# Kernel optimization log

Hardware: AMD Instinct MI355X
Metric: run time of the kernel (lower is better)

Reference implementation:

```python
import jax, jax.numpy as jnp
import numpy as np

NUM_HEADS = 16
ROPE_THETA = 10000.0


def apply_rope(x):
    # x: (B, H, T, hd), interleaved-pair RoPE (rotary-embedding-torch convention)
    T, hd = x.shape[-2], x.shape[-1]
    inv_freq = 1.0 / (ROPE_THETA ** (jnp.arange(0, hd, 2, dtype=jnp.float32) / hd))  # (hd/2,)
    ang = jnp.arange(T, dtype=jnp.float32)[:, None] * inv_freq[None, :]  # (T, hd/2)
    cos, sin = jnp.cos(ang), jnp.sin(ang)
    x1 = x[..., 0::2]
    x2 = x[..., 1::2]
    r1 = x1 * cos - x2 * sin
    r2 = x1 * sin + x2 * cos
    return jnp.stack([r1, r2], axis=-1).reshape(x.shape)


def setup_inputs() -> dict:
    key = jax.random.key(0)
    ks = jax.random.split(key, 8)
    L, S, B, E = 2048, 2048, 2, 1024
    sc = 1.0 / np.sqrt(E)
    return {
        "query": jax.random.normal(ks[0], (L, B, E), jnp.float32),
        "key": jax.random.normal(ks[1], (S, B, E), jnp.float32),
        "value": jax.random.normal(ks[2], (S, B, E), jnp.float32),
        "key_padding_mask": jnp.zeros((B, S), dtype=bool),
        "Wq": jax.random.normal(ks[3], (E, E), jnp.float32) * sc,
        "bq": jnp.zeros((E,), jnp.float32),
        "Wk": jax.random.normal(ks[4], (E, E), jnp.float32) * sc,
        "bk": jnp.zeros((E,), jnp.float32),
        "Wv": jax.random.normal(ks[5], (E, E), jnp.float32) * sc,
        "bv": jnp.zeros((E,), jnp.float32),
        "Wo": jax.random.normal(ks[6], (E, E), jnp.float32) * sc,
        "bo": jnp.zeros((E,), jnp.float32),
    }


def reference(query, key, value, key_padding_mask, Wq, bq, Wk, bk, Wv, bv, Wo, bo):
    L, B, E = query.shape
    S = key.shape[0]
    H = NUM_HEADS
    hd = E // H
    # projections (torch Linear: x @ W.T + b)
    Q = query @ Wq.T + bq  # (L, B, E)
    K = key @ Wk.T + bk    # (S, B, E)
    V = value @ Wv.T + bv  # (S, B, E)
    # (T, B, E) -> (B, H, T, hd)
    Q = Q.reshape(L, B, H, hd).transpose(1, 2, 0, 3)
    K = K.reshape(S, B, H, hd).transpose(1, 2, 0, 3)
    V = V.reshape(S, B, H, hd).transpose(1, 2, 0, 3)
    Q = apply_rope(Q)
    K = apply_rope(K)
    scores = jnp.einsum("bhld,bhsd->bhls", Q, K) / jnp.sqrt(jnp.float32(hd))
    scores = jnp.where(key_padding_mask[:, None, None, :], -jnp.inf, scores)
    attn = jax.nn.softmax(scores, axis=-1)
    out = jnp.einsum("bhls,bhsd->bhld", attn, V)  # (B, H, L, hd)
    out = out.transpose(2, 0, 1, 3).reshape(L, B, E)
    return out @ Wo.T + bo
```

## Files before the change

### kernel.cpp

```cpp
#include <hip/hip_runtime.h>
#include <hip/hip_bf16.h>

typedef __hip_bfloat16 bf16;
typedef short bf16x8 __attribute__((ext_vector_type(8)));
typedef float f32x4 __attribute__((ext_vector_type(4)));
typedef short s4 __attribute__((ext_vector_type(4)));

#define LL 2048
#define SS 2048
#define EE 1024
#define HH 16
#define HD 64
#define MM (LL * 2)

static __device__ __forceinline__ short f2bs(float f) {
  bf16 h = __float2bfloat16(f);
  short u;
  __builtin_memcpy(&u, &h, 2);
  return u;
}

#define GLL16(gp, lp) __builtin_amdgcn_global_load_lds(                        \
    (const __attribute__((address_space(1))) void*)(gp),                       \
    (__attribute__((address_space(3))) void*)(lp), 16, 0, 0)

__global__ __launch_bounds__(256) void tables_kernel(
    float2* __restrict__ tab, const unsigned char* __restrict__ m,
    float* __restrict__ mf) {
  if (blockIdx.x < 256) {
    int i = blockIdx.x * 256 + threadIdx.x;
    int pos = i >> 5, fi = i & 31;
    float freq = expf(-(float)fi * (9.210340371976184f / 32.0f));
    float ang = (float)pos * freq;
    float s, c;
    sincosf(ang, &s, &c);
    tab[i] = make_float2(c, s);
  } else {
    int i = (blockIdx.x - 256) * 256 + threadIdx.x;
    if (i < 2 * SS) mf[i] = m[i] ? -1e30f : 0.f;
  }
}

__global__ __launch_bounds__(256) void cvt_kernel(const float* __restrict__ src,
                                                  bf16* __restrict__ dst) {
  size_t i = ((size_t)blockIdx.x * 256 + threadIdx.x) * 4;
  float4 v = *(const float4*)(src + i);
  s4 p;
  p[0] = f2bs(v.x); p[1] = f2bs(v.y); p[2] = f2bs(v.z); p[3] = f2bs(v.w);
  *(s4*)(dst + i) = p;
}

__global__ __launch_bounds__(256) void cvt4_kernel(
    const float* __restrict__ s0, const float* __restrict__ s1,
    const float* __restrict__ s2, const float* __restrict__ s3,
    bf16* __restrict__ dst) {
  int sel = blockIdx.x >> 10;
  const float* src = (sel == 0) ? s0 : (sel == 1) ? s1 : (sel == 2) ? s2 : s3;
  size_t loc = ((size_t)(blockIdx.x & 1023) * 256 + threadIdx.x) * 4;
  float4 v = *(const float4*)(src + loc);
  s4 p;
  p[0] = f2bs(v.x); p[1] = f2bs(v.y); p[2] = f2bs(v.z); p[3] = f2bs(v.w);
  *(s4*)(dst + (size_t)sel * EE * EE + loc) = p;
}

template<int MODE, bool XB16, bool WB16>
__global__ __launch_bounds__(256) void proj_kernel(
    const void* __restrict__ Xv, const void* __restrict__ Wv,
    const float* __restrict__ bias, void* __restrict__ dstv,
    const float2* __restrict__ tab)
{
  const int w = threadIdx.x >> 6;
  const int lane = threadIdx.x & 63;
  const int l15 = lane & 15, quad = lane >> 4;
  const int tm = blockIdx.x * 128 + w * 32;
  const int tn = blockIdx.y * 64;

  const size_t aoff0 = (size_t)(tm + l15) * EE + quad * 8;
  const size_t aoff1 = aoff0 + (size_t)16 * EE;
  const size_t woff  = (size_t)(tn + l15) * EE + quad * 8;

  f32x4 zero4 = {0.f, 0.f, 0.f, 0.f};
  f32x4 acc[2][4];
#pragma unroll
  for (int mi = 0; mi < 2; ++mi)
#pragma unroll
    for (int ni = 0; ni < 4; ++ni) acc[mi][ni] = zero4;

  for (int k0 = 0; k0 < EE; k0 += 32) {
    bf16x8 a0, a1;
    if (XB16 || MODE == 3) {
      const bf16* Xb = (const bf16*)Xv;
      a0 = *(const bf16x8*)(Xb + aoff0 + k0);
      a1 = *(const bf16x8*)(Xb + aoff1 + k0);
    } else {
      const float* Xf = (const float*)Xv;
#pragma unroll
      for (int j = 0; j < 8; ++j) a0[j] = f2bs(Xf[aoff0 + k0 + j]);
#pragma unroll
      for (int j = 0; j < 8; ++j) a1[j] = f2bs(Xf[aoff1 + k0 + j]);
    }
#pragma unroll
    for (int ni = 0; ni < 4; ++ni) {
      bf16x8 bv;
      if (WB16) {
        const bf16* Wb = (const bf16*)Wv;
        bv = *(const bf16x8*)(Wb + woff + (size_t)ni * 16 * EE + k0);
      } else {
        const float* Wf = (const float*)Wv;
#pragma unroll
        for (int j = 0; j < 8; ++j) bv[j] = f2bs(Wf[woff + (size_t)ni * 16 * EE + k0 + j]);
      }
      acc[0][ni] = __builtin_amdgcn_mfma_f32_16x16x32_bf16(a0, bv, acc[0][ni], 0, 0, 0);
      acc[1][ni] = __builtin_amdgcn_mfma_f32_16x16x32_bf16(a1, bv, acc[1][ni], 0, 0, 0);
    }
  }

  float bz[4];
#pragma unroll
  for (int ni = 0; ni < 4; ++ni) bz[ni] = bias[tn + ni * 16 + l15];

#pragma unroll
  for (int mi = 0; mi < 2; ++mi) {
#pragma unroll
    for (int ni = 0; ni < 4; ++ni) {
      const int n = tn + ni * 16 + l15;
#pragma unroll
      for (int r = 0; r < 4; ++r) {
        const int m = tm + mi * 16 + quad * 4 + r;
        float v = acc[mi][ni][r] + bz[ni];
        if (MODE <= 1) {
          float other = __shfl_xor(v, 1, 64);
          int pos = m >> 1, b = m & 1, d = n & 63, h = n >> 6;
          float2 cs = tab[pos * 32 + (d >> 1)];
          float rv = (d & 1) ? (other * cs.y + v * cs.x) : (v * cs.x - other * cs.y);
          ((bf16*)dstv)[((size_t)(b * HH + h) * LL + pos) * HD + d] = __float2bfloat16(rv);
        } else if (MODE == 2) {
          int pos = m >> 1, b = m & 1, d = n & 63, h = n >> 6;
          ((bf16*)dstv)[((size_t)(b * HH + h) * HD + d) * SS + pos] = __float2bfloat16(v);
        } else {
          ((float*)dstv)[(size_t)m * EE + n] = v;
        }
      }
    }
  }
}

template<int MODE>
__global__ __launch_bounds__(256) void projs_kernel(
    const bf16* __restrict__ X, const bf16* __restrict__ W,
    const float* __restrict__ bias, void* __restrict__ dstv,
    const float2* __restrict__ tab)
{
  __shared__ __align__(16) bf16 As[2][128 * 64];
  __shared__ __align__(16) bf16 Bs[2][64 * 64];

  const int tid = threadIdx.x;
  const int w = tid >> 6;
  const int lane = tid & 63;
  const int l15 = lane & 15, quad = lane >> 4;
  const int tmb = blockIdx.x * 128;
  const int tm  = tmb + w * 32;
  const int tn  = blockIdx.y * 64;

  const int srow = lane >> 3;
  const int sgc  = ((lane & 7) ^ srow) * 8;

#define PSTAGE(buf, K0) {                                                      \
    _Pragma("unroll")                                                          \
    for (int i = 0; i < 4; ++i) {                                              \
      const int rb = w * 32 + i * 8;                                           \
      GLL16(X + (size_t)(tmb + rb + srow) * EE + (K0) + sgc,                   \
            (bf16*)&As[buf][rb * 64] + lane * 8);                              \
    }                                                                          \
    _Pragma("unroll")                                                          \
    for (int i = 0; i < 2; ++i) {                                              \
      const int rb = w * 16 + i * 8;                                           \
      GLL16(W + (size_t)(tn + rb + srow) * EE + (K0) + sgc,                    \
            (bf16*)&Bs[buf][rb * 64] + lane * 8);                              \
    }                                                                          \
  }

  f32x4 zero4 = {0.f, 0.f, 0.f, 0.f};
  f32x4 acc[2][4];
#pragma unroll
  for (int mi = 0; mi < 2; ++mi)
#pragma unroll
    for (int ni = 0; ni < 4; ++ni) acc[mi][ni] = zero4;

  PSTAGE(0, 0);
  __syncthreads();

  for (int t = 0; t < EE / 64; ++t) {
    const int cur = t & 1;
    if (t + 1 < EE / 64) PSTAGE(cur ^ 1, (t + 1) * 64);
#pragma unroll
    for (int ks = 0; ks < 2; ++ks) {
      const int rsw = ((ks * 4 + quad) ^ (l15 & 7)) * 8;
      bf16x8 a0 = *(const bf16x8*)(&As[cur][0] + (w * 32 + l15) * 64 + rsw);
      bf16x8 a1 = *(const bf16x8*)(&As[cur][0] + (w * 32 + 16 + l15) * 64 + rsw);
#pragma unroll
      for (int ni = 0; ni < 4; ++ni) {
        bf16x8 bfr = *(const bf16x8*)(&Bs[cur][0] + (ni * 16 + l15) * 64 + rsw);
        acc[0][ni] = __builtin_amdgcn_mfma_f32_16x16x32_bf16(a0, bfr, acc[0][ni], 0, 0, 0);
        acc[1][ni] = __builtin_amdgcn_mfma_f32_16x16x32_bf16(a1, bfr, acc[1][ni], 0, 0, 0);
      }
    }
    __syncthreads();
  }
#undef PSTAGE

  float bz[4];
#pragma unroll
  for (int ni = 0; ni < 4; ++ni) bz[ni] = bias[tn + ni * 16 + l15];

#pragma unroll
  for (int mi = 0; mi < 2; ++mi) {
#pragma unroll
    for (int ni = 0; ni < 4; ++ni) {
      const int n = tn + ni * 16 + l15;
#pragma unroll
      for (int r = 0; r < 4; ++r) {
        const int m = tm + mi * 16 + quad * 4 + r;
        float v = acc[mi][ni][r] + bz[ni];
        if (MODE <= 1) {
          float other = __shfl_xor(v, 1, 64);
          int pos = m >> 1, b = m & 1, d = n & 63, h = n >> 6;
          float2 cs = tab[pos * 32 + (d >> 1)];
          float rv = (d & 1) ? (other * cs.y + v * cs.x) : (v * cs.x - other * cs.y);
          ((bf16*)dstv)[((size_t)(b * HH + h) * LL + pos) * HD + d] = __float2bfloat16(rv);
        } else if (MODE == 2) {
          int pos = m >> 1, b = m & 1, d = n & 63, h = n >> 6;
          ((bf16*)dstv)[((size_t)(b * HH + h) * HD + d) * SS + pos] = __float2bfloat16(v);
        } else {
          ((float*)dstv)[(size_t)m * EE + n] = v;
        }
      }
    }
  }
}

__global__ __launch_bounds__(256) void attn_kernel(
    const bf16* __restrict__ Qr, const bf16* __restrict__ Kr,
    const bf16* __restrict__ Vt, const float* __restrict__ maskf,
    bf16* __restrict__ ctx)
{
  __shared__ __align__(16) bf16 Ks[2][64 * 64];
  __shared__ __align__(16) bf16 Vs[2][64 * 64];
  __shared__ __align__(16) short Plds[4][32][56];

  const int w = threadIdx.x >> 6;
  const int lane = threadIdx.x & 63;
  const int l15 = lane & 15, quad = lane >> 4;
  const int id = blockIdx.x;
  const int bh = id & 31;
  const int qt = id >> 5;
  const int b = bh >> 4, h = bh & 15;
  const int q0 = qt * 128 + w * 32;

  const bf16* Qbh = Qr + (size_t)bh * LL * HD;
  const bf16* Kbh = Kr + (size_t)bh * SS * HD;
  const bf16* Vbh = Vt + (size_t)bh * HD * SS;
  const float* mrow = maskf + b * SS;

  bf16x8 qf[2][2];
#pragma unroll
  for (int mi = 0; mi < 2; ++mi) {
    const bf16* qp = Qbh + (size_t)(q0 + mi * 16 + l15) * HD + quad * 8;
    qf[mi][0] = *(const bf16x8*)(qp);
    qf[mi][1] = *(const bf16x8*)(qp + 32);
  }

  const int srow = lane >> 3;
  const int gswz = ((lane & 7) ^ srow) * 8;
  const int kswz0 = ((quad    ) ^ (l15 & 7)) * 8;
  const int kswz1 = ((quad + 4) ^ (l15 & 7)) * 8;

#define STAGE(buf, S0) {                                                       \
    _Pragma("unroll")                                                          \
    for (int i = 0; i < 2; ++i) {                                              \
      const int rb = w * 16 + i * 8;                                           \
      GLL16(Kbh + (size_t)((S0) + rb + srow) * HD + gswz,                      \
            (bf16*)&Ks[buf][rb * 64] + lane * 8);                              \
      GLL16(Vbh + (size_t)(rb + srow) * SS + (S0) + gswz,                      \
            (bf16*)&Vs[buf][rb * 64] + lane * 8);                              \
    }                                                                          \
  }

  f32x4 zero4 = {0.f, 0.f, 0.f, 0.f};
  f32x4 o[2][4];
#pragma unroll
  for (int mi = 0; mi < 2; ++mi)
#pragma unroll
    for (int t = 0; t < 4; ++t) o[mi][t] = zero4;
  float ps0 = 0.f, ps1 = 0.f;

  STAGE(0, 0);
  __syncthreads();

  for (int t = 0; t < SS / 64; ++t) {
    const int s0 = t * 64;
    const int cur = t & 1;
    if (t + 1 < SS / 64) STAGE(cur ^ 1, s0 + 64);

#pragma unroll
    for (int ss = 0; ss < 2; ++ss) {
      const bf16* Kb = &Ks[cur][ss * 32 * 64];
      bf16x8 kf00 = *(const bf16x8*)(Kb + (l15)      * 64 + kswz0);
      bf16x8 kf01 = *(const bf16x8*)(Kb + (l15)      * 64 + kswz1);
      bf16x8 kf10 = *(const bf16x8*)(Kb + (16 + l15) * 64 + kswz0);
      bf16x8 kf11 = *(const bf16x8*)(Kb + (16 + l15) * 64 + kswz1);
      bf16x8 vf[4];
#pragma unroll
      for (int tt = 0; tt < 4; ++tt)
        vf[tt] = *(const bf16x8*)(&Vs[cur][0] + (tt * 16 + l15) * 64 +
                                  (((ss * 4 + quad) ^ (l15 & 7)) * 8));
      f32x4 mv0 = *(const f32x4*)(mrow + s0 + ss * 32 + quad * 4);
      f32x4 mv1 = *(const f32x4*)(mrow + s0 + ss * 32 + 16 + quad * 4);

#pragma unroll
      for (int mi = 0; mi < 2; ++mi) {
        f32x4 sc0 = zero4, sc1 = zero4;
        sc0 = __builtin_amdgcn_mfma_f32_16x16x32_bf16(kf00, qf[mi][0], sc0, 0, 0, 0);
        sc0 = __builtin_amdgcn_mfma_f32_16x16x32_bf16(kf01, qf[mi][1], sc0, 0, 0, 0);
        sc1 = __builtin_amdgcn_mfma_f32_16x16x32_bf16(kf10, qf[mi][0], sc1, 0, 0, 0);
        sc1 = __builtin_amdgcn_mfma_f32_16x16x32_bf16(kf11, qf[mi][1], sc1, 0, 0, 0);
        s4 pk0, pk1;
#pragma unroll
        for (int r = 0; r < 4; ++r) {
          float p = __expf(sc0[r] * 0.125f + mv0[r]);
          if (mi == 0) ps0 += p; else ps1 += p;
          pk0[r] = f2bs(p);
        }
#pragma unroll
        for (int r = 0; r < 4; ++r) {
          float p = __expf(sc1[r] * 0.125f + mv1[r]);
          if (mi == 0) ps0 += p; else ps1 += p;
          pk1[r] = f2bs(p);
        }
        *(s4*)&Plds[w][mi * 16 + l15][quad * 4] = pk0;
        *(s4*)&Plds[w][mi * 16 + l15][16 + quad * 4] = pk1;
      }
      asm volatile("" ::: "memory");
      bf16x8 pf0 = *(const bf16x8*)&Plds[w][l15][quad * 8];
      bf16x8 pf1 = *(const bf16x8*)&Plds[w][16 + l15][quad * 8];
#pragma unroll
      for (int tt = 0; tt < 4; ++tt) {
        o[0][tt] = __builtin_amdgcn_mfma_f32_16x16x32_bf16(pf0, vf[tt], o[0][tt], 0, 0, 0);
        o[1][tt] = __builtin_amdgcn_mfma_f32_16x16x32_bf16(pf1, vf[tt], o[1][tt], 0, 0, 0);
      }
      asm volatile("" ::: "memory");
    }
    __syncthreads();
  }
#undef STAGE

  float lv0 = ps0; lv0 += __shfl_xor(lv0, 16, 64); lv0 += __shfl_xor(lv0, 32, 64);
  float lv1 = ps1; lv1 += __shfl_xor(lv1, 16, 64); lv1 += __shfl_xor(lv1, 32, 64);

#pragma unroll
  for (int mi = 0; mi < 2; ++mi) {
#pragma unroll
    for (int r = 0; r < 4; ++r) {
      float lv = (mi == 0) ? lv0 : lv1;
      float li = __shfl(lv, quad * 4 + r, 64);
      float inv = 1.0f / li;
      int q = q0 + mi * 16 + quad * 4 + r;
#pragma unroll
      for (int t = 0; t < 4; ++t) {
        float val = o[mi][t][r] * inv;
        ctx[(size_t)(q * 2 + b) * EE + (size_t)h * 64 + t * 16 + l15] = __float2bfloat16(val);
      }
    }
  }
}

extern "C" void kernel_launch(void* const* d_in, const int* in_sizes, int n_in,
                              void* d_out, int out_size, void* d_ws, size_t ws_size,
                              hipStream_t stream) {
  const float* query = (const float*)d_in[0];
  const float* key   = (const float*)d_in[1];
  const float* value = (const float*)d_in[2];
  const unsigned char* mask = (const unsigned char*)d_in[3];
  const float* Wq = (const float*)d_in[4];
  const float* bq = (const float*)d_in[5];
  const float* Wk = (const float*)d_in[6];
  const float* bk = (const float*)d_in[7];
  const float* Wv = (const float*)d_in[8];
  const float* bv = (const float*)d_in[9];
  const float* Wo = (const float*)d_in[10];
  const float* bo = (const float*)d_in[11];

  char* ws = (char*)d_ws;
  const bool big = ws_size >= ((size_t)41 << 20);

  float2* tab   = (float2*)ws;
  float*  maskf = (float*)(ws + (512 << 10));
  bf16* Wb = (bf16*)(ws + ((size_t)1 << 20));
  bf16* Xb = (bf16*)(ws + ((size_t)9 << 20));
  size_t base = big ? ((size_t)17 << 20) : ((size_t)1 << 20);
  bf16* Qr  = (bf16*)(ws + base);
  bf16* Kr  = (bf16*)(ws + base + ((size_t)8 << 20));
  bf16* Vt  = (bf16*)(ws + base + ((size_t)16 << 20));
  bf16* ctx = big ? Xb : (bf16*)(ws + ((size_t)25 << 20));

  tables_kernel<<<272, 256, 0, stream>>>(tab, mask, maskf);

  dim3 gp(MM / 128, EE / 64);
  if (big) {
    cvt4_kernel<<<4096, 256, 0, stream>>>(Wq, Wk, Wv, Wo, Wb);
    cvt_kernel<<<4096, 256, 0, stream>>>(query, Xb);
    projs_kernel<0><<<gp, 256, 0, stream>>>(Xb, Wb, bq, Qr, tab);
    cvt_kernel<<<4096, 256, 0, stream>>>(key, Xb);
    projs_kernel<1><<<gp, 256, 0, stream>>>(Xb, Wb + (size_t)EE * EE, bk, Kr, tab);
    cvt_kernel<<<4096, 256, 0, stream>>>(value, Xb);
    projs_kernel<2><<<gp, 256, 0, stream>>>(Xb, Wb + (size_t)2 * EE * EE, bv, Vt, tab);
  } else {
    proj_kernel<0, false, false><<<gp, 256, 0, stream>>>(query, Wq, bq, Qr, tab);
    proj_kernel<1, false, false><<<gp, 256, 0, stream>>>(key,   Wk, bk, Kr, tab);
    proj_kernel<2, false, false><<<gp, 256, 0, stream>>>(value, Wv, bv, Vt, tab);
  }

  attn_kernel<<<(LL / 128) * 2 * HH, 256, 0, stream>>>(Qr, Kr, Vt, maskf, ctx);

  if (big) projs_kernel<3><<<gp, 256, 0, stream>>>(ctx, Wb + (size_t)3 * EE * EE, bo, d_out, tab);
  else     proj_kernel<3, true, false><<<gp, 256, 0, stream>>>(ctx, Wo, bo, d_out, tab);
}
```

Measured before the change: 265.9 us.

## Fuse fp32-to-bf16 input conversion into a single batched QKV projection kernel

Removes the three separate activation conversion kernels and instead loads fp32 activations directly in the projection, converting to bf16 in registers before storing to LDS. The Q, K and V projections are merged into one 1536-block launch, with K-tile 32 and a launch bound targeting higher occupancy. The output projection gets a new kernel with 64x64 tiles for more blocks. This trades fewer launches and no intermediate bf16 buffer round trip against register-staged fp32 loads, unswizzled LDS layouts that may bank-conflict, and smaller K steps with more barriers.

After: 261.7 us. No clear change (-1.6%).

```diff
diff --git a/kernel.cpp b/kernel.cpp
--- a/kernel.cpp
+++ b/kernel.cpp
@@ -18,6 +18,13 @@
   short u;
   __builtin_memcpy(&u, &h, 2);
   return u;
+}
+
+static __device__ __forceinline__ void st8(bf16* p, float4 x, float4 y) {
+  bf16x8 v;
+  v[0] = f2bs(x.x); v[1] = f2bs(x.y); v[2] = f2bs(x.z); v[3] = f2bs(x.w);
+  v[4] = f2bs(y.x); v[5] = f2bs(y.y); v[6] = f2bs(y.z); v[7] = f2bs(y.w);
+  *(bf16x8*)p = v;
 }
 
 #define GLL16(gp, lp) __builtin_amdgcn_global_load_lds(                        \
@@ -39,15 +46,6 @@
     int i = (blockIdx.x - 256) * 256 + threadIdx.x;
     if (i < 2 * SS) mf[i] = m[i] ? -1e30f : 0.f;
   }
-}
-
-__global__ __launch_bounds__(256) void cvt_kernel(const float* __restrict__ src,
-                                                  bf16* __restrict__ dst) {
-  size_t i = ((size_t)blockIdx.x * 256 + threadIdx.x) * 4;
-  float4 v = *(const float4*)(src + i);
-  s4 p;
-  p[0] = f2bs(v.x); p[1] = f2bs(v.y); p[2] = f2bs(v.z); p[3] = f2bs(v.w);
-  *(s4*)(dst + i) = p;
 }
 
 __global__ __launch_bounds__(256) void cvt4_kernel(
@@ -145,40 +143,37 @@
   }
 }
 
-template<int MODE>
-__global__ __launch_bounds__(256) void projs_kernel(
-    const bf16* __restrict__ X, const bf16* __restrict__ W,
-    const float* __restrict__ bias, void* __restrict__ dstv,
+__global__ __launch_bounds__(256, 4) void qkv_kernel(
+    const float* __restrict__ Xq, const float* __restrict__ Xk,
+    const float* __restrict__ Xv, const bf16* __restrict__ Wb,
+    const float* __restrict__ bq, const float* __restrict__ bk,
+    const float* __restrict__ bv, bf16* __restrict__ Qr,
+    bf16* __restrict__ Kr, bf16* __restrict__ Vt,
     const float2* __restrict__ tab)
 {
-  __shared__ __align__(16) bf16 As[2][128 * 64];
-  __shared__ __align__(16) bf16 Bs[2][64 * 64];
+  __shared__ __align__(16) bf16 As[2][128 * 32];
+  __shared__ __align__(16) bf16 Bs[2][64 * 32];
 
   const int tid = threadIdx.x;
   const int w = tid >> 6;
   const int lane = tid & 63;
   const int l15 = lane & 15, quad = lane >> 4;
-  const int tmb = blockIdx.x * 128;
-  const int tm  = tmb + w * 32;
-  const int tn  = blockIdx.y * 64;
-
-  const int srow = lane >> 3;
-  const int sgc  = ((lane & 7) ^ srow) * 8;
-
-#define PSTAGE(buf, K0) {                                                      \
-    _Pragma("unroll")                                                          \
-    for (int i = 0; i < 4; ++i) {                                              \
-      const int rb = w * 32 + i * 8;                                           \
-      GLL16(X + (size_t)(tmb + rb + srow) * EE + (K0) + sgc,                   \
-            (bf16*)&As[buf][rb * 64] + lane * 8);                              \
-    }                                                                          \
-    _Pragma("unroll")                                                          \
-    for (int i = 0; i < 2; ++i) {                                              \
-      const int rb = w * 16 + i * 8;                                           \
-      GLL16(W + (size_t)(tn + rb + srow) * EE + (K0) + sgc,                    \
-            (bf16*)&Bs[buf][rb * 64] + lane * 8);                              \
-    }                                                                          \
-  }
+  const int id = blockIdx.x;
+  const int z = id >> 9;
+  const int g = id & 511;
+  const int tmb = (g & 31) * 128;
+  const int tn  = (g >> 5) * 64;
+
+  const float* Xf = (z == 0) ? Xq : (z == 1) ? Xk : Xv;
+  const bf16* Wm  = Wb + (size_t)z * EE * EE;
+  const float* bias = (z == 0) ? bq : (z == 1) ? bk : bv;
+  bf16* dst = (z == 0) ? Qr : (z == 1) ? Kr : Vt;
+
+  const int ar = tid >> 2;
+  const int ac = (tid & 3) * 8;
+  const float* gA0 = Xf + (size_t)(tmb + ar) * EE + ac;
+  const float* gA1 = gA0 + (size_t)64 * EE;
+  const bf16* gB = Wm + (size_t)(tn + w * 16 + (lane >> 2)) * EE + (lane & 3) * 8;
 
   f32x4 zero4 = {0.f, 0.f, 0.f, 0.f};
   f32x4 acc[2][4];
@@ -187,27 +182,42 @@
 #pragma unroll
     for (int ni = 0; ni < 4; ++ni) acc[mi][ni] = zero4;
 
-  PSTAGE(0, 0);
+  {
+    float4 a00 = *(const float4*)(gA0);
+    float4 a01 = *(const float4*)(gA0 + 4);
+    float4 a10 = *(const float4*)(gA1);
+    float4 a11 = *(const float4*)(gA1 + 4);
+    GLL16(gB, (bf16*)&Bs[0][w * 16 * 32] + lane * 8);
+    st8(&As[0][ar * 32 + ac], a00, a01);
+    st8(&As[0][(64 + ar) * 32 + ac], a10, a11);
+  }
   __syncthreads();
 
-  for (int t = 0; t < EE / 64; ++t) {
+  for (int t = 0; t < 32; ++t) {
     const int cur = t & 1;
-    if (t + 1 < EE / 64) PSTAGE(cur ^ 1, (t + 1) * 64);
-#pragma unroll
-    for (int ks = 0; ks < 2; ++ks) {
-      const int rsw = ((ks * 4 + quad) ^ (l15 & 7)) * 8;
-      bf16x8 a0 = *(const bf16x8*)(&As[cur][0] + (w * 32 + l15) * 64 + rsw);
-      bf16x8 a1 = *(const bf16x8*)(&As[cur][0] + (w * 32 + 16 + l15) * 64 + rsw);
-#pragma unroll
-      for (int ni = 0; ni < 4; ++ni) {
-        bf16x8 bfr = *(const bf16x8*)(&Bs[cur][0] + (ni * 16 + l15) * 64 + rsw);
-        acc[0][ni] = __builtin_amdgcn_mfma_f32_16x16x32_bf16(a0, bfr, acc[0][ni], 0, 0, 0);
-        acc[1][ni] = __builtin_amdgcn_mfma_f32_16x16x32_bf16(a1, bfr, acc[1][ni], 0, 0, 0);
-      }
+    float4 a00, a01, a10, a11;
+    if (t < 31) {
+      const int k0 = (t + 1) * 32;
+      a00 = *(const float4*)(gA0 + k0);
+      a01 = *(const float4*)(gA0 + k0 + 4);
+      a10 = *(const float4*)(gA1 + k0);
+      a11 = *(const float4*)(gA1 + k0 + 4);
+      GLL16(gB + k0, (bf16*)&Bs[cur ^ 1][w * 16 * 32] + lane * 8);
+    }
+    bf16x8 af0 = *(const bf16x8*)(&As[cur][(w * 32 + l15) * 32 + quad * 8]);
+    bf16x8 af1 = *(const bf16x8*)(&As[cur][(w * 32 + 16 + l15) * 32 + quad * 8]);
+#pragma unroll
+    for (int ni = 0; ni < 4; ++ni) {
+      bf16x8 bfr = *(const bf16x8*)(&Bs[cur][(ni * 16 + l15) * 32 + quad * 8]);
+      acc[0][ni] = __builtin_amdgcn_mfma_f32_16x16x32_bf16(af0, bfr, acc[0][ni], 0, 0, 0);
+      acc[1][ni] = __builtin_amdgcn_mfma_f32_16x16x32_bf16(af1, bfr, acc[1][ni], 0, 0, 0);
+    }
+    if (t < 31) {
+      st8(&As[cur ^ 1][ar * 32 + ac], a00, a01);
+      st8(&As[cur ^ 1][(64 + ar) * 32 + ac], a10, a11);
     }
     __syncthreads();
   }
-#undef PSTAGE
 
   float bz[4];
 #pragma unroll
@@ -220,21 +230,76 @@
       const int n = tn + ni * 16 + l15;
 #pragma unroll
       for (int r = 0; r < 4; ++r) {
-        const int m = tm + mi * 16 + quad * 4 + r;
+        const int m = tmb + w * 32 + mi * 16 + quad * 4 + r;
         float v = acc[mi][ni][r] + bz[ni];
-        if (MODE <= 1) {
+        if (z <= 1) {
           float other = __shfl_xor(v, 1, 64);
           int pos = m >> 1, b = m & 1, d = n & 63, h = n >> 6;
           float2 cs = tab[pos * 32 + (d >> 1)];
           float rv = (d & 1) ? (other * cs.y + v * cs.x) : (v * cs.x - other * cs.y);
-          ((bf16*)dstv)[((size_t)(b * HH + h) * LL + pos) * HD + d] = __float2bfloat16(rv);
-        } else if (MODE == 2) {
+          dst[((size_t)(b * HH + h) * LL + pos) * HD + d] = __float2bfloat16(rv);
+        } else {
           int pos = m >> 1, b = m & 1, d = n & 63, h = n >> 6;
-          ((bf16*)dstv)[((size_t)(b * HH + h) * HD + d) * SS + pos] = __float2bfloat16(v);
-        } else {
-          ((float*)dstv)[(size_t)m * EE + n] = v;
+          dst[((size_t)(b * HH + h) * HD + d) * SS + pos] = __float2bfloat16(v);
         }
       }
+    }
+  }
+}
+
+__global__ __launch_bounds__(256) void projo_kernel(
+    const bf16* __restrict__ X, const bf16* __restrict__ W,
+    const float* __restrict__ bias, float* __restrict__ dst)
+{
+  __shared__ __align__(16) bf16 As[2][64 * 32];
+  __shared__ __align__(16) bf16 Bs[2][64 * 32];
+
+  const int tid = threadIdx.x;
+  const int w = tid >> 6;
+  const int lane = tid & 63;
+  const int l15 = lane & 15, quad = lane >> 4;
+  const int tmb = blockIdx.x * 64;
+  const int tn  = blockIdx.y * 64;
+
+  const bf16* gA = X + (size_t)(tmb + w * 16 + (lane >> 2)) * EE + (lane & 3) * 8;
+  const bf16* gB = W + (size_t)(tn  + w * 16 + (lane >> 2)) * EE + (lane & 3) * 8;
+
+  f32x4 zero4 = {0.f, 0.f, 0.f, 0.f};
+  f32x4 acc[4];
+#pragma unroll
+  for (int ni = 0; ni < 4; ++ni) acc[ni] = zero4;
+
+  GLL16(gA, (bf16*)&As[0][w * 16 * 32] + lane * 8);
+  GLL16(gB, (bf16*)&Bs[0][w * 16 * 32] + lane * 8);
+  __syncthreads();
+
+  for (int t = 0; t < 32; ++t) {
+    const int cur = t & 1;
+    if (t < 31) {
+      const int k0 = (t + 1) * 32;
+      GLL16(gA + k0, (bf16*)&As[cur ^ 1][w * 16 * 32] + lane * 8);
+      GLL16(gB + k0, (bf16*)&Bs[cur ^ 1][w * 16 * 32] + lane * 8);
+    }
+    bf16x8 af = *(const bf16x8*)(&As[cur][(w * 16 + l15) * 32 + quad * 8]);
+#pragma unroll
+    for (int ni = 0; ni < 4; ++ni) {
+      bf16x8 bfr = *(const bf16x8*)(&Bs[cur][(ni * 16 + l15) * 32 + quad * 8]);
+      acc[ni] = __builtin_amdgcn_mfma_f32_16x16x32_bf16(af, bfr, acc[ni], 0, 0, 0);
+    }
+    __syncthreads();
+  }
+
+  float bz[4];
+#pragma unroll
+  for (int ni = 0; ni < 4; ++ni) bz[ni] = bias[tn + ni * 16 + l15];
+
+#pragma unroll
+  for (int ni = 0; ni < 4; ++ni) {
+    const int n = tn + ni * 16 + l15;
+#pragma unroll
+    for (int r = 0; r < 4; ++r) {
+      const int m = tmb + w * 16 + quad * 4 + r;
+      dst[(size_t)m * EE + n] = acc[ni][r] + bz[ni];
     }
   }
 }
@@ -396,25 +461,20 @@
   float2* tab   = (float2*)ws;
   float*  maskf = (float*)(ws + (512 << 10));
   bf16* Wb = (bf16*)(ws + ((size_t)1 << 20));
-  bf16* Xb = (bf16*)(ws + ((size_t)9 << 20));
-  size_t base = big ? ((size_t)17 << 20) : ((size_t)1 << 20);
+  size_t base = big ? ((size_t)9 << 20) : ((size_t)1 << 20);
   bf16* Qr  = (bf16*)(ws + base);
   bf16* Kr  = (bf16*)(ws + base + ((size_t)8 << 20));
   bf16* Vt  = (bf16*)(ws + base + ((size_t)16 << 20));
-  bf16* ctx = big ? Xb : (bf16*)(ws + ((size_t)25 << 20));
+  bf16* ctx = (bf16*)(ws + base + ((size_t)24 << 20));
 
   tables_kernel<<<272, 256, 0, stream>>>(tab, mask, maskf);
 
-  dim3 gp(MM / 128, EE / 64);
   if (big) {
     cvt4_kernel<<<4096, 256, 0, stream>>>(Wq, Wk, Wv, Wo, Wb);
-    cvt_kernel<<<4096, 256, 0, stream>>>(query, Xb);
-    projs_kernel<0><<<gp, 256, 0, stream>>>(Xb, Wb, bq, Qr, tab);
-    cvt_kernel<<<4096, 256, 0, stream>>>(key, Xb);
-    projs_kernel<1><<<gp, 256, 0, stream>>>(Xb, Wb + (size_t)EE * EE, bk, Kr, tab);
-    cvt_kernel<<<4096, 256, 0, stream>>>(value, Xb);
-    projs_kernel<2><<<gp, 256, 0, stream>>>(Xb, Wb + (size_t)2 * EE * EE, bv, Vt, tab);
+    qkv_kernel<<<1536, 256, 0, stream>>>(query, key, value, Wb, bq, bk, bv,
+                                         Qr, Kr, Vt, tab);
   } else {
+    dim3 gp(MM / 128, EE / 64);
     proj_kernel<0, false, false><<<gp, 256, 0, stream>>>(query, Wq, bq, Qr, tab);
     proj_kernel<1, false, false><<<gp, 256, 0, stream>>>(key,   Wk, bk, Kr, tab);
     proj_kernel<2, false, false><<<gp, 256, 0, stream>>>(value, Wv, bv, Vt, tab);
@@ -422,6 +482,11 @@
 
   attn_kernel<<<(LL / 128) * 2 * HH, 256, 0, stream>>>(Qr, Kr, Vt, maskf, ctx);
 
-  if (big) projs_kernel<3><<<gp, 256, 0, stream>>>(ctx, Wb + (size_t)3 * EE * EE, bo, d_out, tab);
-  else     proj_kernel<3, true, false><<<gp, 256, 0, stream>>>(ctx, Wo, bo, d_out, tab);
-}
+  if (big) {
+    dim3 go(MM / 64, EE / 64);
+    projo_kernel<<<go, 256, 0, stream>>>(ctx, Wb + (size_t)3 * EE * EE, bo, (float*)d_out);
+  } else {
+    dim3 gp(MM / 128, EE / 64);
+    proj_kernel<3, true, false><<<gp, 256, 0, stream>>>(ctx, Wo, bo, d_out, tab);
+  }
+}
```
